# Kernel optimization log

Measured on AMD Instinct MI355X. Metric: run time of the kernel, lower is better.

The kernel has to match this reference:

```python
import jax, jax.numpy as jnp
import numpy as np

NEG_SLOPE = 0.2

def gat_conv(x, edge_index, W, a_src, a_dst, b, heads, out_ch, concat):
    # PyG GATConv (add_self_loops=True, eval mode / no dropout)
    N = x.shape[0]
    loop = jnp.arange(N, dtype=edge_index.dtype)
    src = jnp.concatenate([edge_index[0], loop])
    dst = jnp.concatenate([edge_index[1], loop])
    h = (x @ W.T).reshape(N, heads, out_ch)            # [N,H,C]
    alpha_s = (h * a_src).sum(-1)                      # [N,H]
    alpha_d = (h * a_dst).sum(-1)                      # [N,H]
    e = jax.nn.leaky_relu(alpha_s[src] + alpha_d[dst], NEG_SLOPE)  # [E,H]
    # segment softmax over incoming edges of each dst node
    m = jax.ops.segment_max(e, dst, num_segments=N)
    e = jnp.exp(e - m[dst])
    denom = jax.ops.segment_sum(e, dst, num_segments=N)
    alpha = e / (denom[dst] + 1e-16)                   # [E,H]
    msg = h[src] * alpha[..., None]                    # [E,H,C]
    out = jax.ops.segment_sum(msg, dst, num_segments=N)  # [N,H,C]
    out = out.reshape(N, heads * out_ch) if concat else out.mean(axis=1)
    return out + b


def setup_inputs() -> dict:
    key = jax.random.key(0)
    ks = jax.random.split(key, 16)
    N, E, F_in, HID, H, OUT = 20000, 320000, 512, 256, 8, 128
    C = HID // H  # 32 channels per head
    x = jax.random.normal(ks[0], (N, F_in), dtype=jnp.float32)
    edge_index = jax.random.randint(ks[1], (2, E), 0, N, dtype=jnp.int32)
    s = 0.05
    inp = {
        'x': x, 'edge_index': edge_index,
        # layer 0: F_in -> H*C, concat
        'W0': jax.random.normal(ks[2], (H * C, F_in)) * s,
        'a_src0': jax.random.normal(ks[3], (1, H, C)) * s,
        'a_dst0': jax.random.normal(ks[4], (1, H, C)) * s,
        'b0': jnp.zeros((H * C,), jnp.float32),
        # layer 1: H*C -> H*C, concat
        'W1': jax.random.normal(ks[5], (H * C, H * C)) * s,
        'a_src1': jax.random.normal(ks[6], (1, H, C)) * s,
        'a_dst1': jax.random.normal(ks[7], (1, H, C)) * s,
        'b1': jnp.zeros((H * C,), jnp.float32),
        # layer 2: H*C -> OUT, 1 head, concat=False
        'W2': jax.random.normal(ks[8], (OUT, H * C)) * s,
        'a_src2': jax.random.normal(ks[9], (1, 1, OUT)) * s,
        'a_dst2': jax.random.normal(ks[10], (1, 1, OUT)) * s,
        'b2': jnp.zeros((OUT,), jnp.float32),
    }
    return inp


def reference(x, edge_index, W0, a_src0, a_dst0, b0, W1, a_src1, a_dst1, b1,
              W2, a_src2, a_dst2, b2):
    H, C, OUT = 8, 32, 128
    h = gat_conv(x, edge_index, W0, a_src0, a_dst0, b0, H, C, True)
    h = jax.nn.relu(h)
    h = gat_conv(h, edge_index, W1, a_src1, a_dst1, b1, H, C, True)
    h = jax.nn.relu(h)
    h_pen = h  # h_list[-1]
    h = gat_conv(h, edge_index, W2, a_src2, a_dst2, b2, 1, OUT, False)
    return (h_pen, h)
```

## Files before the change

### kernel.cpp

```cpp
#include <hip/hip_runtime.h>
#include <hip/hip_bf16.h>


using bf16 = __hip_bfloat16;

typedef __attribute__((ext_vector_type(8))) short bf16x8;
typedef __attribute__((ext_vector_type(4))) short short4v;
typedef __attribute__((ext_vector_type(4))) float f32x4;
typedef __attribute__((ext_vector_type(2))) float f32x2;
typedef __attribute__((ext_vector_type(2))) unsigned int uint2v;

__device__ __forceinline__ float u2f(unsigned u) { union { float f; unsigned u; } c; c.u = u; return c.f; }
__device__ __forceinline__ unsigned f2u(float x) { union { float f; unsigned u; } c; c.f = x; return c.u; }
__device__ __forceinline__ short bfbits(float x) {
  unsigned xu = f2u(x);
  return (short)((xu + 0x7FFF + ((xu >> 16) & 1)) >> 16);
}

__global__ void hist_kernel(const int* __restrict__ ei, int E, int N, int* __restrict__ cnt) {
  int e = blockIdx.x * 256 + threadIdx.x;
  if (e >= E + N) return;
  int dst = (e < E) ? ei[E + e] : (e - E);
  atomicAdd(&cnt[dst], 1);
}

__global__ __launch_bounds__(1024) void scan_kernel(const int* __restrict__ cnt,
                                                    int* __restrict__ row_start, int N) {
  __shared__ int part[1024];
  int t = threadIdx.x;
  int chunk = (N + 1023) / 1024;
  int lo = t * chunk; if (lo > N) lo = N;
  int hi = lo + chunk; if (hi > N) hi = N;
  int s = 0;
  for (int i = lo; i < hi; ++i) s += cnt[i];
  part[t] = s;
  __syncthreads();
  for (int off = 1; off < 1024; off <<= 1) {
    int add = (t >= off) ? part[t - off] : 0;
    __syncthreads();
    part[t] += add;
    __syncthreads();
  }
  int run = part[t] - s;
  for (int i = lo; i < hi; ++i) { row_start[i] = run; run += cnt[i]; }
  if (t == 1023) row_start[N] = part[1023];
}

__global__ void scatter_kernel(const int* __restrict__ ei, int E, int N,
                               const int* __restrict__ row_start, int* __restrict__ cursor,
                               int* __restrict__ csr_src) {
  int e = blockIdx.x * 256 + threadIdx.x;
  if (e >= E + N) return;
  int src, dst;
  if (e < E) { src = ei[e]; dst = ei[E + e]; }
  else       { src = e - E; dst = e - E; }
  int pos = atomicAdd(&cursor[dst], 1);
  csr_src[row_start[dst] + pos] = src;
}

__global__ void split3_kernel(const float* __restrict__ W0, const float* __restrict__ W1,
                              const float* __restrict__ W2,
                              unsigned short* __restrict__ W0h, unsigned short* __restrict__ W0l,
                              unsigned short* __restrict__ W1h, unsigned short* __restrict__ W1l,
                              unsigned short* __restrict__ W2h, unsigned short* __restrict__ W2l,
                              int n0_4, int n1_4, int n2_4) {
  int i = blockIdx.x * 256 + threadIdx.x;
  const float* in; unsigned short *hi, *lo; int idx;
  if (i < n0_4)                { in = W0; hi = W0h; lo = W0l; idx = i; }
  else if (i < n0_4 + n1_4)    { in = W1; hi = W1h; lo = W1l; idx = i - n0_4; }
  else if (i < n0_4 + n1_4 + n2_4) { in = W2; hi = W2h; lo = W2l; idx = i - n0_4 - n1_4; }
  else return;
  f32x4 v = *(const f32x4*)(in + (size_t)idx * 4);
  short4v h, l;
#pragma unroll
  for (int k = 0; k < 4; ++k) {
    short hb = bfbits(v[k]);
    h[k] = hb;
    l[k] = bfbits(v[k] - u2f(((unsigned)(unsigned short)hb) << 16));
  }
  *(short4v*)(hi + (size_t)idx * 4) = h;
  *(short4v*)(lo + (size_t)idx * 4) = l;
}

__global__ void prefrag_kernel(const unsigned short* __restrict__ Wh0, const unsigned short* __restrict__ Wl0,
                               const unsigned short* __restrict__ Wh1, const unsigned short* __restrict__ Wl1,
                               const unsigned short* __restrict__ Wh2, const unsigned short* __restrict__ Wl2,
                               unsigned short* __restrict__ F0h, unsigned short* __restrict__ F0l,
                               unsigned short* __restrict__ F1h, unsigned short* __restrict__ F1l,
                               unsigned short* __restrict__ F2h, unsigned short* __restrict__ F2l,
                               int c0, int c1, int c2) {
  int id = blockIdx.x * 256 + threadIdx.x;
  const unsigned short *Wh, *Wl; unsigned short *Fh, *Fl; int K, ktmax, rid;
  if (id < c0)            { Wh = Wh0; Wl = Wl0; Fh = F0h; Fl = F0l; K = 512; ktmax = 16; rid = id; }
  else if (id < c0 + c1)  { Wh = Wh1; Wl = Wl1; Fh = F1h; Fl = F1l; K = 256; ktmax = 8;  rid = id - c0; }
  else if (id < c0 + c1 + c2) { Wh = Wh2; Wl = Wl2; Fh = F2h; Fl = F2l; K = 256; ktmax = 8; rid = id - c0 - c1; }
  else return;
  int lane = rid & 63;
  int blk  = rid >> 6;
  int jb   = blk / ktmax;
  int kt32 = blk % ktmax;
  int lr = lane & 15, g = lane >> 4;
  int col = jb * 16 + lr;
  const unsigned short* sh = Wh + (size_t)col * K + kt32 * 32;
  const unsigned short* sl = Wl + (size_t)col * K + kt32 * 32;
  short4v h0, h1, l0, l1;
#pragma unroll
  for (int e = 0; e < 4; ++e) {
    h0[e] = sh[g * 4 + e];      h1[e] = sh[16 + g * 4 + e];
    l0[e] = sl[g * 4 + e];      l1[e] = sl[16 + g * 4 + e];
  }
  size_t o = ((size_t)blk * 64 + lane) * 8;
  *(short4v*)(Fh + o)     = h0;
  *(short4v*)(Fh + o + 4) = h1;
  *(short4v*)(Fl + o)     = l0;
  *(short4v*)(Fl + o + 4) = l1;
}

__global__ void zero2_f32_kernel(float* __restrict__ a, float* __restrict__ b, int n) {
  int i = blockIdx.x * 256 + threadIdx.x;
  if (i < n) a[i] = 0.f;
  else if (i < 2 * n) b[i - n] = 0.f;
}

#define LDP 40

__device__ __forceinline__ bf16x8 make_frag(const short* S, int row, int g) {
  short4v klo = *(const short4v*)&S[row * LDP + g * 4];
  short4v khi = *(const short4v*)&S[row * LDP + 16 + g * 4];
  bf16x8 r;
#pragma unroll
  for (int i = 0; i < 4; ++i) { r[i] = klo[i]; r[i + 4] = khi[i]; }
  return r;
}

template <bool FUSE8, bool FUSE1>
__global__ __launch_bounds__(256) void gemm_mfma(const float* __restrict__ Af,
                                                 const unsigned short* __restrict__ Fh,
                                                 const unsigned short* __restrict__ Fl,
                                                 const float* __restrict__ Asrc,
                                                 const float* __restrict__ Adst,
                                                 float* __restrict__ as_,
                                                 float* __restrict__ ad_,
                                                 unsigned short* __restrict__ C16,
                                                 int M, int Nn, int K, int NB) {
  int id = blockIdx.x;
  int r8 = id & 7;
  int q  = id >> 3;
  int bn = q % NB;
  int bm = r8 + 8 * (q / NB);
  if (bm * 64 >= M) return;

  __shared__ short Ah[64 * LDP];
  __shared__ short Al[64 * LDP];
  int t = threadIdx.x;
  int w = t >> 6, l = t & 63;
  int g = l >> 4, lr = l & 15;
  int ktmax = K >> 5;

  f32x4 acc[4];
#pragma unroll
  for (int j = 0; j < 4; ++j) acc[j] = (f32x4)(0.f);

  int srow = t >> 2;
  int sseg = (t & 3) * 8;
  int gm = bm * 64 + srow;
  const float* Abase = Af + (size_t)gm * K + sseg;
  const unsigned short* FhL = Fh + (size_t)l * 8;
  const unsigned short* FlL = Fl + (size_t)l * 8;

  f32x4 va0 = (f32x4)(0.f), va1 = (f32x4)(0.f);
  if (gm < M) { va0 = *(const f32x4*)(Abase); va1 = *(const f32x4*)(Abase + 4); }

  for (int kt32 = 0; kt32 < ktmax; ++kt32) {
    short4v h0, l0, h1, l1;
#pragma unroll
    for (int i = 0; i < 4; ++i) {
      short hb0 = bfbits(va0[i]);
      l0[i] = bfbits(va0[i] - u2f(((unsigned)(unsigned short)hb0) << 16));
      h0[i] = hb0;
      short hb1 = bfbits(va1[i]);
      l1[i] = bfbits(va1[i] - u2f(((unsigned)(unsigned short)hb1) << 16));
      h1[i] = hb1;
    }
    __syncthreads();
    *(short4v*)&Ah[srow * LDP + sseg]     = h0;
    *(short4v*)&Ah[srow * LDP + sseg + 4] = h1;
    *(short4v*)&Al[srow * LDP + sseg]     = l0;
    *(short4v*)&Al[srow * LDP + sseg + 4] = l1;
    __syncthreads();

    if (kt32 + 1 < ktmax) {
      int k2 = (kt32 + 1) << 5;
      if (gm < M) { va0 = *(const f32x4*)(Abase + k2); va1 = *(const f32x4*)(Abase + k2 + 4); }
    }

    int arow = w * 16 + lr;
    bf16x8 ah = make_frag(Ah, arow, g);
    bf16x8 al = make_frag(Al, arow, g);
#pragma unroll
    for (int j = 0; j < 4; ++j) {
      size_t fo = ((size_t)((bn * 4 + j) * ktmax + kt32) * 64) * 8;
      bf16x8 bh = *(const bf16x8*)(FhL + fo);
      bf16x8 bl = *(const bf16x8*)(FlL + fo);
      acc[j] = __builtin_amdgcn_mfma_f32_16x16x32_bf16(ah, bh, acc[j], 0, 0, 0);
      acc[j] = __builtin_amdgcn_mfma_f32_16x16x32_bf16(al, bh, acc[j], 0, 0, 0);
      acc[j] = __builtin_amdgcn_mfma_f32_16x16x32_bf16(ah, bl, acc[j], 0, 0, 0);
    }
  }

#pragma unroll
  for (int j = 0; j < 4; ++j) {
#pragma unroll
    for (int r = 0; r < 4; ++r) {
      int row = bm * 64 + w * 16 + g * 4 + r;
      int col = bn * 64 + j * 16 + lr;
      if (row < M) C16[(size_t)row * Nn + col] = (unsigned short)bfbits(acc[j][r]);
    }
  }

  if constexpr (FUSE8) {
    float cs[4], cd[4];
#pragma unroll
    for (int j = 0; j < 4; ++j) {
      cs[j] = Asrc[bn * 64 + j * 16 + lr];
      cd[j] = Adst[bn * 64 + j * 16 + lr];
    }
#pragma unroll
    for (int r = 0; r < 4; ++r) {
      float sA0 = acc[0][r] * cs[0] + acc[1][r] * cs[1];
      float sA1 = acc[2][r] * cs[2] + acc[3][r] * cs[3];
      float sD0 = acc[0][r] * cd[0] + acc[1][r] * cd[1];
      float sD1 = acc[2][r] * cd[2] + acc[3][r] * cd[3];
#pragma unroll
      for (int mask = 1; mask < 16; mask <<= 1) {
        sA0 += __shfl_xor(sA0, mask);
        sA1 += __shfl_xor(sA1, mask);
        sD0 += __shfl_xor(sD0, mask);
        sD1 += __shfl_xor(sD1, mask);
      }
      if (lr == 0) {
        int row = bm * 64 + w * 16 + g * 4 + r;
        if (row < M) {
          as_[row * 8 + bn * 2]     = sA0;
          as_[row * 8 + bn * 2 + 1] = sA1;
          ad_[row * 8 + bn * 2]     = sD0;
          ad_[row * 8 + bn * 2 + 1] = sD1;
        }
      }
    }
  }

  if constexpr (FUSE1) {
    float cs[4], cd[4];
#pragma unroll
    for (int j = 0; j < 4; ++j) {
      cs[j] = Asrc[bn * 64 + j * 16 + lr];
      cd[j] = Adst[bn * 64 + j * 16 + lr];
    }
#pragma unroll
    for (int r = 0; r < 4; ++r) {
      float sA = acc[0][r] * cs[0] + acc[1][r] * cs[1] + acc[2][r] * cs[2] + acc[3][r] * cs[3];
      float sD = acc[0][r] * cd[0] + acc[1][r] * cd[1] + acc[2][r] * cd[2] + acc[3][r] * cd[3];
#pragma unroll
      for (int mask = 1; mask < 16; mask <<= 1) {
        sA += __shfl_xor(sA, mask);
        sD += __shfl_xor(sD, mask);
      }
      if (lr == 0) {
        int row = bm * 64 + w * 16 + g * 4 + r;
        if (row < M) {
          atomicAdd(&as_[row], sA);
          atomicAdd(&ad_[row], sD);
        }
      }
    }
  }
}

template <int H, int C, bool RELU>
__global__ __launch_bounds__(64) void agg_kernel(const unsigned short* __restrict__ Hb16,
                                                 const float* __restrict__ as_,
                                                 const float* __restrict__ ad_,
                                                 const int* __restrict__ row_start,
                                                 const int* __restrict__ csr_src,
                                                 const float* __restrict__ bias,
                                                 float* __restrict__ out, int N) {
  int n = blockIdx.x;
  if (n >= N) return;
  int l = threadIdx.x;
  int s = row_start[n], e = row_start[n + 1];

  constexpr int LPH = 64 / H;
  constexpr int CPL = C / LPH;
  constexpr int HC = H * C;
  int h2 = l / LPH;
  int cb = (l % LPH) * CPL;
  float ad2 = ad_[n * H + h2];

  float acc[CPL];
#pragma unroll
  for (int c = 0; c < CPL; ++c) acc[c] = 0.f;
  float denom = 0.f;

  auto lrelu = [](float x) { return x > 0.f ? x : 0.2f * x; };

  int j = s;
  for (; j + 3 < e; j += 4) {
    int s0 = csr_src[j], s1 = csr_src[j + 1], s2 = csr_src[j + 2], s3 = csr_src[j + 3];
    float x0 = as_[s0 * H + h2], x1 = as_[s1 * H + h2];
    float x2 = as_[s2 * H + h2], x3 = as_[s3 * H + h2];
    const unsigned short* hp0 = Hb16 + (size_t)s0 * HC + h2 * C + cb;
    const unsigned short* hp1 = Hb16 + (size_t)s1 * HC + h2 * C + cb;
    const unsigned short* hp2 = Hb16 + (size_t)s2 * HC + h2 * C + cb;
    const unsigned short* hp3 = Hb16 + (size_t)s3 * HC + h2 * C + cb;
    float p0 = __expf(lrelu(x0 + ad2)), p1 = __expf(lrelu(x1 + ad2));
    float p2 = __expf(lrelu(x2 + ad2)), p3 = __expf(lrelu(x3 + ad2));
    denom += (p0 + p1) + (p2 + p3);
    if constexpr (CPL == 4) {
      uint2v u0 = *(const uint2v*)hp0;
      uint2v u1 = *(const uint2v*)hp1;
      uint2v u2 = *(const uint2v*)hp2;
      uint2v u3 = *(const uint2v*)hp3;
#pragma unroll
      for (int c = 0; c < 2; ++c) {
        acc[2 * c]     += p0 * u2f(u0[c] << 16)         + p1 * u2f(u1[c] << 16)
                        + p2 * u2f(u2[c] << 16)         + p3 * u2f(u3[c] << 16);
        acc[2 * c + 1] += p0 * u2f(u0[c] & 0xFFFF0000u) + p1 * u2f(u1[c] & 0xFFFF0000u)
                        + p2 * u2f(u2[c] & 0xFFFF0000u) + p3 * u2f(u3[c] & 0xFFFF0000u);
      }
    } else {
      unsigned u0 = *(const unsigned*)hp0;
      unsigned u1 = *(const unsigned*)hp1;
      unsigned u2 = *(const unsigned*)hp2;
      unsigned u3 = *(const unsigned*)hp3;
      acc[0] += p0 * u2f(u0 << 16)         + p1 * u2f(u1 << 16)
              + p2 * u2f(u2 << 16)         + p3 * u2f(u3 << 16);
      acc[1] += p0 * u2f(u0 & 0xFFFF0000u) + p1 * u2f(u1 & 0xFFFF0000u)
              + p2 * u2f(u2 & 0xFFFF0000u) + p3 * u2f(u3 & 0xFFFF0000u);
    }
  }
  for (; j < e; ++j) {
    int s0 = csr_src[j];
    float p0 = __expf(lrelu(as_[s0 * H + h2] + ad2));
    denom += p0;
    const unsigned short* hp0 = Hb16 + (size_t)s0 * HC + h2 * C + cb;
    if constexpr (CPL == 4) {
      uint2v u0 = *(const uint2v*)hp0;
#pragma unroll
      for (int c = 0; c < 2; ++c) {
        acc[2 * c]     += p0 * u2f(u0[c] << 16);
        acc[2 * c + 1] += p0 * u2f(u0[c] & 0xFFFF0000u);
      }
    } else {
      unsigned u0 = *(const unsigned*)hp0;
      acc[0] += p0 * u2f(u0 << 16);
      acc[1] += p0 * u2f(u0 & 0xFFFF0000u);
    }
  }

  float inv = 1.f / (denom + 1e-16f);
#pragma unroll
  for (int c = 0; c < CPL; ++c) {
    float v = acc[c] * inv + bias[h2 * C + cb + c];
    if (RELU) v = fmaxf(v, 0.f);
    out[(size_t)n * HC + h2 * C + cb + c] = v;
  }
}

extern "C" void kernel_launch(void* const* d_in, const int* in_sizes, int n_in,
                              void* d_out, int out_size, void* d_ws, size_t ws_size,
                              hipStream_t stream) {
  const float* x    = (const float*)d_in[0];
  const int*   ei   = (const int*)d_in[1];
  const float* W0   = (const float*)d_in[2];
  const float* asr0 = (const float*)d_in[3];
  const float* adt0 = (const float*)d_in[4];
  const float* b0   = (const float*)d_in[5];
  const float* W1   = (const float*)d_in[6];
  const float* asr1 = (const float*)d_in[7];
  const float* adt1 = (const float*)d_in[8];
  const float* b1   = (const float*)d_in[9];
  const float* W2   = (const float*)d_in[10];
  const float* asr2 = (const float*)d_in[11];
  const float* adt2 = (const float*)d_in[12];
  const float* b2   = (const float*)d_in[13];

  const int FIN = 512, HID = 256, OUTC = 128;
  int N = in_sizes[0] / FIN;
  int E = in_sizes[1] / 2;
  int Etot = E + N;

  char* ws = (char*)d_ws;
  size_t off = 0;
  auto alloc = [&](size_t bytes) -> void* {
    void* p = ws + off;
    off = (off + bytes + 255) & ~(size_t)255;
    return p;
  };
  int* cnt       = (int*)alloc((size_t)N * 4);
  int* cursor    = (int*)alloc((size_t)N * 4);
  int* row_start = (int*)alloc((size_t)(N + 1) * 4);
  int* csr_src   = (int*)alloc((size_t)Etot * 4);
  float* as_     = (float*)alloc((size_t)N * 8 * 4);
  float* ad_     = (float*)alloc((size_t)N * 8 * 4);
  unsigned short* Hb16 = (unsigned short*)alloc((size_t)N * HID * 2);
  float* act     = (float*)alloc((size_t)N * HID * 4);
  unsigned short* W0h = (unsigned short*)alloc((size_t)HID * FIN * 2);
  unsigned short* W0l = (unsigned short*)alloc((size_t)HID * FIN * 2);
  unsigned short* W1h = (unsigned short*)alloc((size_t)HID * HID * 2);
  unsigned short* W1l = (unsigned short*)alloc((size_t)HID * HID * 2);
  unsigned short* W2h = (unsigned short*)alloc((size_t)OUTC * HID * 2);
  unsigned short* W2l = (unsigned short*)alloc((size_t)OUTC * HID * 2);
  unsigned short* F0h = (unsigned short*)alloc((size_t)HID * FIN * 2);
  unsigned short* F0l = (unsigned short*)alloc((size_t)HID * FIN * 2);
  unsigned short* F1h = (unsigned short*)alloc((size_t)HID * HID * 2);
  unsigned short* F1l = (unsigned short*)alloc((size_t)HID * HID * 2);
  unsigned short* F2h = (unsigned short*)alloc((size_t)OUTC * HID * 2);
  unsigned short* F2l = (unsigned short*)alloc((size_t)OUTC * HID * 2);

  float* hpen = (float*)d_out;
  float* out2 = (float*)d_out + (size_t)N * HID;

  int n0_4 = HID * FIN / 4, n1_4 = HID * HID / 4, n2_4 = OUTC * HID / 4;
  int nsplit = n0_4 + n1_4 + n2_4;
  split3_kernel<<<(nsplit + 255) / 256, 256, 0, stream>>>(W0, W1, W2, W0h, W0l, W1h, W1l,
                                                          W2h, W2l, n0_4, n1_4, n2_4);
  int c0 = (HID / 16) * (FIN / 32) * 64;
  int c1 = (HID / 16) * (HID / 32) * 64;
  int c2 = (OUTC / 16) * (HID / 32) * 64;
  prefrag_kernel<<<(c0 + c1 + c2 + 255) / 256, 256, 0, stream>>>(
      W0h, W0l, W1h, W1l, W2h, W2l, F0h, F0l, F1h, F1l, F2h, F2l, c0, c1, c2);

  (void)hipMemsetAsync(cnt, 0, (size_t)((char*)cursor - (char*)cnt) + (size_t)N * 4, stream);
  int eb = (Etot + 255) / 256;
  hist_kernel<<<eb, 256, 0, stream>>>(ei, E, N, cnt);
  scan_kernel<<<1, 1024, 0, stream>>>(cnt, row_start, N);
  scatter_kernel<<<eb, 256, 0, stream>>>(ei, E, N, row_start, cursor, csr_src);

  int mb = (N + 63) / 64;
  int mb8 = (mb + 7) / 8;
  int grid4 = 8 * 4 * mb8;
  int grid2 = 8 * 2 * mb8;

  gemm_mfma<true, false><<<grid4, 256, 0, stream>>>(x, F0h, F0l, asr0, adt0, as_, ad_,
                                                    Hb16, N, HID, FIN, 4);
  agg_kernel<8, 32, true><<<N, 64, 0, stream>>>(Hb16, as_, ad_, row_start, csr_src, b0,
                                                act, N);

  gemm_mfma<true, false><<<grid4, 256, 0, stream>>>(act, F1h, F1l, asr1, adt1, as_, ad_,
                                                    Hb16, N, HID, HID, 4);
  agg_kernel<8, 32, true><<<N, 64, 0, stream>>>(Hb16, as_, ad_, row_start, csr_src, b1,
                                                hpen, N);

  zero2_f32_kernel<<<(2 * N + 255) / 256, 256, 0, stream>>>(as_, ad_, N);
  gemm_mfma<false, true><<<grid2, 256, 0, stream>>>(hpen, F2h, F2l, asr2, adt2, as_, ad_,
                                                    Hb16, N, OUTC, HID, 2);
  agg_kernel<1, 128, false><<<N, 64, 0, stream>>>(Hb16, as_, ad_, row_start, csr_src, b2,
                                                  out2, N);
}
```

Before: 223.1 us.

## Fuse weight split into prefrag, stage GEMM output via LDS, pack 4 nodes per agg block

The separate weight hi/lo split kernel is folded into the fragment-prep kernel, which now reads the fp32 weights directly. This removes one launch and the intermediate buffers. The GEMM epilogue writes bf16 results to shared memory first and then stores each row with 16-byte vector writes, replacing scattered 2-byte global stores. The aggregation kernel now runs four 64-lane node workers per 256-thread block instead of one node per 64-thread block, which cuts the block count and scheduling overhead. All three layers use the new paths.

```diff
diff --git a/kernel.cpp b/kernel.cpp
--- a/kernel.cpp
+++ b/kernel.cpp
@@ -7,7 +7,6 @@
 typedef __attribute__((ext_vector_type(8))) short bf16x8;
 typedef __attribute__((ext_vector_type(4))) short short4v;
 typedef __attribute__((ext_vector_type(4))) float f32x4;
-typedef __attribute__((ext_vector_type(2))) float f32x2;
 typedef __attribute__((ext_vector_type(2))) unsigned int uint2v;
 
 __device__ __forceinline__ float u2f(unsigned u) { union { float f; unsigned u; } c; c.u = u; return c.f; }
@@ -58,56 +57,33 @@
   csr_src[row_start[dst] + pos] = src;
 }
 
-__global__ void split3_kernel(const float* __restrict__ W0, const float* __restrict__ W1,
-                              const float* __restrict__ W2,
-                              unsigned short* __restrict__ W0h, unsigned short* __restrict__ W0l,
-                              unsigned short* __restrict__ W1h, unsigned short* __restrict__ W1l,
-                              unsigned short* __restrict__ W2h, unsigned short* __restrict__ W2l,
-                              int n0_4, int n1_4, int n2_4) {
-  int i = blockIdx.x * 256 + threadIdx.x;
-  const float* in; unsigned short *hi, *lo; int idx;
-  if (i < n0_4)                { in = W0; hi = W0h; lo = W0l; idx = i; }
-  else if (i < n0_4 + n1_4)    { in = W1; hi = W1h; lo = W1l; idx = i - n0_4; }
-  else if (i < n0_4 + n1_4 + n2_4) { in = W2; hi = W2h; lo = W2l; idx = i - n0_4 - n1_4; }
-  else return;
-  f32x4 v = *(const f32x4*)(in + (size_t)idx * 4);
-  short4v h, l;
-#pragma unroll
-  for (int k = 0; k < 4; ++k) {
-    short hb = bfbits(v[k]);
-    h[k] = hb;
-    l[k] = bfbits(v[k] - u2f(((unsigned)(unsigned short)hb) << 16));
-  }
-  *(short4v*)(hi + (size_t)idx * 4) = h;
-  *(short4v*)(lo + (size_t)idx * 4) = l;
-}
-
-__global__ void prefrag_kernel(const unsigned short* __restrict__ Wh0, const unsigned short* __restrict__ Wl0,
-                               const unsigned short* __restrict__ Wh1, const unsigned short* __restrict__ Wl1,
-                               const unsigned short* __restrict__ Wh2, const unsigned short* __restrict__ Wl2,
+__global__ void prefrag_kernel(const float* __restrict__ W0, const float* __restrict__ W1,
+                               const float* __restrict__ W2,
                                unsigned short* __restrict__ F0h, unsigned short* __restrict__ F0l,
                                unsigned short* __restrict__ F1h, unsigned short* __restrict__ F1l,
                                unsigned short* __restrict__ F2h, unsigned short* __restrict__ F2l,
                                int c0, int c1, int c2) {
   int id = blockIdx.x * 256 + threadIdx.x;
-  const unsigned short *Wh, *Wl; unsigned short *Fh, *Fl; int K, ktmax, rid;
-  if (id < c0)            { Wh = Wh0; Wl = Wl0; Fh = F0h; Fl = F0l; K = 512; ktmax = 16; rid = id; }
-  else if (id < c0 + c1)  { Wh = Wh1; Wl = Wl1; Fh = F1h; Fl = F1l; K = 256; ktmax = 8;  rid = id - c0; }
-  else if (id < c0 + c1 + c2) { Wh = Wh2; Wl = Wl2; Fh = F2h; Fl = F2l; K = 256; ktmax = 8; rid = id - c0 - c1; }
+  const float* W; unsigned short *Fh, *Fl; int K, ktmax, rid;
+  if (id < c0)                { W = W0; Fh = F0h; Fl = F0l; K = 512; ktmax = 16; rid = id; }
+  else if (id < c0 + c1)      { W = W1; Fh = F1h; Fl = F1l; K = 256; ktmax = 8;  rid = id - c0; }
+  else if (id < c0 + c1 + c2) { W = W2; Fh = F2h; Fl = F2l; K = 256; ktmax = 8;  rid = id - c0 - c1; }
   else return;
   int lane = rid & 63;
   int blk  = rid >> 6;
   int jb   = blk / ktmax;
   int kt32 = blk % ktmax;
   int lr = lane & 15, g = lane >> 4;
-  int col = jb * 16 + lr;
-  const unsigned short* sh = Wh + (size_t)col * K + kt32 * 32;
-  const unsigned short* sl = Wl + (size_t)col * K + kt32 * 32;
+  const float* s = W + (size_t)(jb * 16 + lr) * K + kt32 * 32;
   short4v h0, h1, l0, l1;
 #pragma unroll
   for (int e = 0; e < 4; ++e) {
-    h0[e] = sh[g * 4 + e];      h1[e] = sh[16 + g * 4 + e];
-    l0[e] = sl[g * 4 + e];      l1[e] = sl[16 + g * 4 + e];
+    float a = s[g * 4 + e];
+    short hb = bfbits(a);
+    h0[e] = hb; l0[e] = bfbits(a - u2f(((unsigned)(unsigned short)hb) << 16));
+    float b = s[16 + g * 4 + e];
+    short hb2 = bfbits(b);
+    h1[e] = hb2; l1[e] = bfbits(b - u2f(((unsigned)(unsigned short)hb2) << 16));
   }
   size_t o = ((size_t)blk * 64 + lane) * 8;
   *(short4v*)(Fh + o)     = h0;
@@ -152,6 +128,7 @@
 
   __shared__ short Ah[64 * LDP];
   __shared__ short Al[64 * LDP];
+  __shared__ short CT[4][16][64];
   int t = threadIdx.x;
   int w = t >> 6, l = t & 63;
   int g = l >> 4, lr = l & 15;
@@ -209,12 +186,20 @@
   }
 
 #pragma unroll
-  for (int j = 0; j < 4; ++j) {
-#pragma unroll
-    for (int r = 0; r < 4; ++r) {
-      int row = bm * 64 + w * 16 + g * 4 + r;
-      int col = bn * 64 + j * 16 + lr;
-      if (row < M) C16[(size_t)row * Nn + col] = (unsigned short)bfbits(acc[j][r]);
+  for (int j = 0; j < 4; ++j)
+#pragma unroll
+    for (int r = 0; r < 4; ++r)
+      CT[w][g * 4 + r][j * 16 + lr] = bfbits(acc[j][r]);
+  {
+    int rrow = l >> 2, rseg = l & 3;
+    int grow = bm * 64 + w * 16 + rrow;
+    if (grow < M) {
+      const short* src = &CT[w][rrow][rseg * 16];
+      uint4 v0 = *(const uint4*)(src);
+      uint4 v1 = *(const uint4*)(src + 8);
+      unsigned short* dst = C16 + (size_t)grow * Nn + bn * 64 + rseg * 16;
+      *(uint4*)dst = v0;
+      *(uint4*)(dst + 8) = v1;
     }
   }
 
@@ -278,16 +263,16 @@
 }
 
 template <int H, int C, bool RELU>
-__global__ __launch_bounds__(64) void agg_kernel(const unsigned short* __restrict__ Hb16,
-                                                 const float* __restrict__ as_,
-                                                 const float* __restrict__ ad_,
-                                                 const int* __restrict__ row_start,
-                                                 const int* __restrict__ csr_src,
-                                                 const float* __restrict__ bias,
-                                                 float* __restrict__ out, int N) {
-  int n = blockIdx.x;
+__global__ __launch_bounds__(256) void agg_kernel(const unsigned short* __restrict__ Hb16,
+                                                  const float* __restrict__ as_,
+                                                  const float* __restrict__ ad_,
+                                                  const int* __restrict__ row_start,
+                                                  const int* __restrict__ csr_src,
+                                                  const float* __restrict__ bias,
+                                                  float* __restrict__ out, int N) {
+  int n = blockIdx.x * 4 + (threadIdx.x >> 6);
   if (n >= N) return;
-  int l = threadIdx.x;
+  int l = threadIdx.x & 63;
   int s = row_start[n], e = row_start[n + 1];
 
   constexpr int LPH = 64 / H;
@@ -405,12 +390,6 @@
   float* ad_     = (float*)alloc((size_t)N * 8 * 4);
   unsigned short* Hb16 = (unsigned short*)alloc((size_t)N * HID * 2);
   float* act     = (float*)alloc((size_t)N * HID * 4);
-  unsigned short* W0h = (unsigned short*)alloc((size_t)HID * FIN * 2);
-  unsigned short* W0l = (unsigned short*)alloc((size_t)HID * FIN * 2);
-  unsigned short* W1h = (unsigned short*)alloc((size_t)HID * HID * 2);
-  unsigned short* W1l = (unsigned short*)alloc((size_t)HID * HID * 2);
-  unsigned short* W2h = (unsigned short*)alloc((size_t)OUTC * HID * 2);
-  unsigned short* W2l = (unsigned short*)alloc((size_t)OUTC * HID * 2);
   unsigned short* F0h = (unsigned short*)alloc((size_t)HID * FIN * 2);
   unsigned short* F0l = (unsigned short*)alloc((size_t)HID * FIN * 2);
   unsigned short* F1h = (unsigned short*)alloc((size_t)HID * HID * 2);
@@ -421,15 +400,11 @@
   float* hpen = (float*)d_out;
   float* out2 = (float*)d_out + (size_t)N * HID;
 
-  int n0_4 = HID * FIN / 4, n1_4 = HID * HID / 4, n2_4 = OUTC * HID / 4;
-  int nsplit = n0_4 + n1_4 + n2_4;
-  split3_kernel<<<(nsplit + 255) / 256, 256, 0, stream>>>(W0, W1, W2, W0h, W0l, W1h, W1l,
-                                                          W2h, W2l, n0_4, n1_4, n2_4);
   int c0 = (HID / 16) * (FIN / 32) * 64;
   int c1 = (HID / 16) * (HID / 32) * 64;
   int c2 = (OUTC / 16) * (HID / 32) * 64;
   prefrag_kernel<<<(c0 + c1 + c2 + 255) / 256, 256, 0, stream>>>(
-      W0h, W0l, W1h, W1l, W2h, W2l, F0h, F0l, F1h, F1l, F2h, F2l, c0, c1, c2);
+      W0, W1, W2, F0h, F0l, F1h, F1l, F2h, F2l, c0, c1, c2);
 
   (void)hipMemsetAsync(cnt, 0, (size_t)((char*)cursor - (char*)cnt) + (size_t)N * 4, stream);
   int eb = (Etot + 255) / 256;
@@ -441,20 +416,21 @@
   int mb8 = (mb + 7) / 8;
   int grid4 = 8 * 4 * mb8;
   int grid2 = 8 * 2 * mb8;
+  int gagg = (N + 3) / 4;
 
   gemm_mfma<true, false><<<grid4, 256, 0, stream>>>(x, F0h, F0l, asr0, adt0, as_, ad_,
                                                     Hb16, N, HID, FIN, 4);
-  agg_kernel<8, 32, true><<<N, 64, 0, stream>>>(Hb16, as_, ad_, row_start, csr_src, b0,
-                                                act, N);
+  agg_kernel<8, 32, true><<<gagg, 256, 0, stream>>>(Hb16, as_, ad_, row_start, csr_src, b0,
+                                                    act, N);
 
   gemm_mfma<true, false><<<grid4, 256, 0, stream>>>(act, F1h, F1l, asr1, adt1, as_, ad_,
                                                     Hb16, N, HID, HID, 4);
-  agg_kernel<8, 32, true><<<N, 64, 0, stream>>>(Hb16, as_, ad_, row_start, csr_src, b1,
-                                                hpen, N);
+  agg_kernel<8, 32, true><<<gagg, 256, 0, stream>>>(Hb16, as_, ad_, row_start, csr_src, b1,
+                                                    hpen, N);
 
   zero2_f32_kernel<<<(2 * N + 255) / 256, 256, 0, stream>>>(as_, ad_, N);
   gemm_mfma<false, true><<<grid2, 256, 0, stream>>>(hpen, F2h, F2l, asr2, adt2, as_, ad_,
                                                     Hb16, N, OUTC, HID, 2);
-  agg_kernel<1, 128, false><<<N, 64, 0, stream>>>(Hb16, as_, ad_, row_start, csr_src, b2,
-                                                  out2, N);
-}
+  agg_kernel<1, 128, false><<<gagg, 256, 0, stream>>>(Hb16, as_, ad_, row_start, csr_src, b2,
+                                                      out2, N);
+}
```

New measurement: 229.1 us. 2.7% more time.
